# Optimization experiments

Measured on AMD Instinct MI355X. Metric: run time of the kernel, lower is better.

## Reference

```python
import jax, jax.numpy as jnp
import numpy as np

# Irreps 0e+1o+2e+3o: (name, dim); total irreps dim D = 1+3+5+7 = 16
IRS = [("0e", 1), ("1o", 3), ("2e", 5), ("3o", 7)]
D = 16
# path multiplicities per correlation order (MACE-like)
MULS = {3: [5, 8, 10, 10], 2: [2, 3, 4, 4], 1: [1, 1, 1, 1]}
NUM_RBF = 32
CHANNELS = 128
NUM_SPECIES = 64
BATCH = 256


def _make_U():
    # Sparse Clebsch-Gordan-like basis tensors: shape (D,)*order + (mul, ir_dim).
    # Stand-in for e3nn.reduced_symmetric_tensor_product_basis: deterministic,
    rng = np.random.default_rng(42)
    U = {}
    for order in (3, 2, 1):
        for (ir, dim), mul in zip(IRS, MULS[order]):
            shape = (D,) * order + (mul, dim)
            dense = rng.standard_normal(shape).astype(np.float32)
            mask = (rng.random(shape) < 0.1).astype(np.float32)
            U[(order, ir)] = jnp.asarray(dense * mask)
    return U

U_BASIS = _make_U()
WKEYS = [(o, ir) for o in (3, 2, 1) for ir, _ in IRS]


def setup_inputs() -> dict:
    key = jax.random.key(0)
    ks = jax.random.split(key, 16)
    inp = {
        "x": jax.random.normal(ks[0], (BATCH, CHANNELS, D), dtype=jnp.float32),
        "index": jax.random.randint(ks[1], (BATCH,), 0, NUM_SPECIES),
        "embed_table": jax.random.normal(ks[2], (NUM_SPECIES, NUM_RBF), dtype=jnp.float32),
    }
    i = 3
    for order in (3, 2, 1):
        for (ir, _), mul in zip(IRS, MULS[order]):
            inp[f"w{order}_{ir}"] = jax.random.normal(ks[i], (NUM_RBF, mul, CHANNELS), dtype=jnp.float32)
            i += 1
    return inp


def _forward(x, species_ind, Wd):
    # x: (b, c, D); species_ind: (b, num_rbf); Wd[(order, ir)]: (num_rbf, mul, c)
    out = {}
    fresh = set()
    for order in (3, 2, 1):
        for ir, _ in IRS:
            u = U_BASIS[(order, ir)] / order  # ((D,)*order, mul, ir_dim)
            # species-gathered per-channel path weights: (b, mul, c)
            w = jnp.einsum('be,ekc->bkc', species_ind, Wd[(order, ir)])
            if ir not in out:
                # highest order: contract one D axis with x, mul with w
                out[ir] = jnp.einsum('...jki,bkc,bcj->bc...i', u, w, x)
                fresh.add(ir)
            else:
                out[ir] = out[ir] + jnp.einsum('...ki,bkc->bc...i', u, w)
        for ir, _ in IRS:
            if ir in fresh:
                fresh.discard(ir)
                continue
            # contract one more D axis against x after each lower order
            out[ir] = jnp.einsum('bc...ji,bcj->bc...i', out[ir], x)
    # final per-ir shape (b, c, ir_dim); concat -> (b, c, D)
    return jnp.concatenate([out[ir] for ir, _ in IRS], axis=-1)


def reference(x, index, embed_table, w3_0e, w3_1o, w3_2e, w3_3o, w2_0e, w2_1o, w2_2e, w2_3o, w1_0e, w1_1o, w1_2e, w1_3o):
    ws = (w3_0e, w3_1o, w3_2e, w3_3o, w2_0e, w2_1o, w2_2e, w2_3o, w1_0e, w1_1o, w1_2e, w1_3o)
    Wd = {k: w for k, w in zip(WKEYS, ws)}
    species_ind = embed_table[index]  # (b, num_rbf) embedding lookup
    return _forward(x, species_ind, Wd)
```

## Files before the change

### kernel.cpp

```cpp
#include <hip/hip_runtime.h>
#include <cstdint>
#include <cmath>
#include <cstring>

#define D16    16
#define CH     128
#define NBATCH 256
#define NSP    64
#define NRBF   32
#define NKK    50
#define NT3    816
#define NT2    136
#define LD3    160
#define LD2    64
#define U3_FLOATS (NT3*LD3)
#define U2_FLOATS (NT2*LD2)
#define U1_FLOATS 256
#define U_TOTAL   (U3_FLOATS+U2_FLOATS+U1_FLOATS)

#define KPAD   1024
#define NPAD   256
#define NCH_REAL 61
#define RING   3

typedef __attribute__((ext_vector_type(8)))  short short8;
typedef __attribute__((ext_vector_type(16))) float f32x16;

__device__ uint16_t g_B[NPAD*KPAD];
__device__ float    g_ws[NSP*NKK*CH];
__device__ float    g_part[NBATCH*2*CH*D16];

__device__ __constant__ int8_t KK_ARR[NKK] = {
  0,0,0,0,0, 1,1,1,1,1,1,1,1, 2,2,2,2,2,2,2,2,2,2, 3,3,3,3,3,3,3,3,3,3,
  4,4, 5,5,5, 6,6,6,6, 7,7,7,7, 8,9,10,11 };
__device__ __constant__ int8_t KK_K[NKK] = {
  0,1,2,3,4, 0,1,2,3,4,5,6,7, 0,1,2,3,4,5,6,7,8,9, 0,1,2,3,4,5,6,7,8,9,
  0,1, 0,1,2, 0,1,2,3, 0,1,2,3, 0,0,0,0 };
__device__ __constant__ int8_t ARR_MUL[12] = {5,8,10,10, 2,3,4,4, 1,1,1,1};

struct WPtrs { const float* p[12]; };

struct TTab { uint8_t a0[KPAD]; uint8_t a1[KPAD]; uint8_t a2[KPAD]; };
constexpr TTab make_tab() {
  TTab t{};
  int i = 0;
  for (int A = 0; A < 16; ++A)
    for (int B = A; B < 16; ++B)
      for (int C = B; C < 16; ++C) { t.a0[i]=(uint8_t)A; t.a1[i]=(uint8_t)B; t.a2[i]=(uint8_t)C; ++i; }
  for (int A = 0; A < 16; ++A)
    for (int B = A; B < 16; ++B) { t.a0[i]=(uint8_t)A; t.a1[i]=(uint8_t)B; t.a2[i]=16; ++i; }
  for (int A = 0; A < 16; ++A) { t.a0[i]=(uint8_t)A; t.a1[i]=16; t.a2[i]=16; ++i; }
  for (; i < KPAD; ++i) { t.a0[i]=17; t.a1[i]=17; t.a2[i]=17; }
  return t;
}
static constexpr TTab TT = make_tab();

template<int K>
__device__ __forceinline__ float featK(const float (&xv)[16]) {
  constexpr int A = TT.a0[K], B = TT.a1[K], C = TT.a2[K];
  if constexpr (A == 17) { return 0.f; }
  else {
    float m = xv[A];
    if constexpr (B < 16) m *= xv[B];
    if constexpr (C < 16) m *= xv[C];
    return m;
  }
}

template<int K0>
__device__ __forceinline__ uint32_t pack2(const float (&xv)[16]) {
  if constexpr (TT.a0[K0] == 17 && TT.a0[K0+1] == 17) { return 0u; }
  else {
    float lo = featK<K0>(xv);
    float hi = featK<K0+1>(xv);
    uint32_t d;
    asm("v_cvt_pk_bf16_f32 %0, %1, %2" : "=v"(d) : "v"(lo), "v"(hi));
    return d;
  }
}

template<int CHUNK>
__device__ __forceinline__ short8 build_frag(const float (&xv)[16], bool kg_hi) {
  uint32_t pk0 = pack2<CHUNK*16 + 0>(xv);
  uint32_t pk1 = pack2<CHUNK*16 + 2>(xv);
  uint32_t pk2 = pack2<CHUNK*16 + 4>(xv);
  uint32_t pk3 = pack2<CHUNK*16 + 6>(xv);
  uint32_t pk4 = pack2<CHUNK*16 + 8>(xv);
  uint32_t pk5 = pack2<CHUNK*16 + 10>(xv);
  uint32_t pk6 = pack2<CHUNK*16 + 12>(xv);
  uint32_t pk7 = pack2<CHUNK*16 + 14>(xv);
  union { uint32_t u[4]; short8 s; } r;
  r.u[0] = kg_hi ? pk4 : pk0;
  r.u[1] = kg_hi ? pk5 : pk1;
  r.u[2] = kg_hi ? pk6 : pk2;
  r.u[3] = kg_hi ? pk7 : pk3;
  return r.s;
}

__device__ uint32_t colpack(int cc) {
  int kk, ii;
  if (cc < 149) {
    if (cc < 5)       { kk = cc;               ii = 0; }
    else if (cc < 29) { int r = cc-5;  kk = 5  + r/3; ii = 1 + r%3; }
    else if (cc < 79) { int r = cc-29; kk = 13 + r/5; ii = 4 + r%5; }
    else              { int r = cc-79; kk = 23 + r/7; ii = 9 + r%7; }
  } else if (cc < 208) {
    int j = cc - 149;
    if (j < 2)        { kk = 33 + j;           ii = 0; }
    else if (j < 11)  { int r = j-2;  kk = 35 + r/3; ii = 1 + r%3; }
    else if (j < 31)  { int r = j-11; kk = 38 + r/5; ii = 4 + r%5; }
    else              { int r = j-31; kk = 42 + r/7; ii = 9 + r%7; }
  } else {
    int j = cc - 208;
    if (j < 1)        { kk = 46; ii = 0; }
    else if (j < 4)   { kk = 47; ii = j; }
    else if (j < 9)   { kk = 48; ii = j; }
    else              { kk = 49; ii = j; }
  }
  return (uint32_t)((kk<<4) | ii);
}

__global__ void weights_kernel(const float* __restrict__ embed, WPtrs wp) {
  int kk = blockIdx.x;
  int s  = blockIdx.y;
  int c  = threadIdx.x;
  int ai = KK_ARR[kk];
  int k  = KK_K[kk];
  int mul = ARR_MUL[ai];
  const float* __restrict__ W = wp.p[ai];
  float a = 0.f;
  #pragma unroll 8
  for (int e = 0; e < NRBF; ++e)
    a = fmaf(embed[s*NRBF + e], W[(e*mul + k)*CH + c], a);
  g_ws[(s*NKK + kk)*CH + c] = a;
}

template<int C>
__device__ __forceinline__ void kstep(const float (&xv)[16], bool kg_hi,
                                      const uint16_t* __restrict__ pB,
                                      uint4 (&br0)[RING], uint4 (&br1)[RING],
                                      f32x16& a0, f32x16& a1) {
  union UU { uint4 u; short8 s; };
  UU b0; b0.u = br0[C % RING];
  UU b1; b1.u = br1[C % RING];
  short8 af = build_frag<C>(xv, kg_hi);
  a0 = __builtin_amdgcn_mfma_f32_32x32x16_bf16(af, b0.s, a0, 0, 0, 0);
  a1 = __builtin_amdgcn_mfma_f32_32x32x16_bf16(af, b1.s, a1, 0, 0, 0);
  if constexpr (C + RING < NCH_REAL) {
    br0[C % RING] = *(const uint4*)(pB + (size_t)(C+RING)*4096);
    br1[C % RING] = *(const uint4*)(pB + (size_t)(C+RING)*4096 + 256);
  }
}

__global__ __launch_bounds__(512, 2) void main_kernel(const float* __restrict__ x,
                                                      const int* __restrict__ index) {
  __shared__ float    out_lds[128*18];
  __shared__ uint32_t tab2[256];

  const int tid  = threadIdx.x;
  const int lane = tid & 63;
  const int l31  = lane & 31;
  const int kg   = lane >> 5;
  const bool kg_hi = (kg != 0);
  const int w    = tid >> 6;
  const int wmg  = w >> 1;
  const int wq   = w & 1;
  const int b    = blockIdx.x;
  const int nh   = blockIdx.y;
  const int s    = index[b];

  const int r0 = wmg*32 + l31;
  float xv[16];
  {
    const float4* xs = (const float4*)(x + ((size_t)b*CH + r0)*D16);
    #pragma unroll
    for (int qq = 0; qq < 4; ++qq) {
      float4 v = xs[qq];
      xv[qq*4+0]=v.x; xv[qq*4+1]=v.y; xv[qq*4+2]=v.z; xv[qq*4+3]=v.w;
    }
  }

  for (int i = tid; i < 128*18; i += 512) out_lds[i] = 0.f;
  if (tid < 256) tab2[tid] = (tid < 224) ? colpack(tid) : 0u;

  const uint16_t* __restrict__ pB = g_B + ((size_t)kg*256 + nh*128 + wq*64 + l31)*8;

  uint4 br0[RING], br1[RING];
  #pragma unroll
  for (int c = 0; c < RING; ++c) {
    br0[c] = *(const uint4*)(pB + (size_t)c*4096);
    br1[c] = *(const uint4*)(pB + (size_t)c*4096 + 256);
  }

  f32x16 a0, a1;
  #pragma unroll
  for (int q = 0; q < 16; ++q) { a0[q]=0.f; a1[q]=0.f; }

#define S1_(C) kstep<(C)>(xv, kg_hi, pB, br0, br1, a0, a1);
#define S4_(C) S1_(C) S1_(C+1) S1_(C+2) S1_(C+3)
  S4_(0)  S4_(4)  S4_(8)  S4_(12) S4_(16) S4_(20) S4_(24) S4_(28)
  S4_(32) S4_(36) S4_(40) S4_(44) S4_(48) S4_(52) S4_(56) S1_(60)
#undef S4_
#undef S1_

  __syncthreads();

#define FOLD(ACC, NT) { \
    int col = nh*128 + wq*64 + (NT)*32 + l31; \
    if (col < 224) { \
      uint32_t v = tab2[col]; \
      int kk = v >> 4, ii = v & 15; \
      const float* wsrow = g_ws + ((size_t)s*NKK + kk)*CH + wmg*32; \
      _Pragma("unroll") \
      for (int qg = 0; qg < 4; ++qg) { \
        int rlb = 8*qg + 4*kg; \
        float4 wv = *(const float4*)(wsrow + rlb); \
        int rbase = wmg*32 + rlb; \
        atomicAdd(&out_lds[(rbase + 0)*18 + ii], wv.x * (ACC)[qg*4+0]); \
        atomicAdd(&out_lds[(rbase + 1)*18 + ii], wv.y * (ACC)[qg*4+1]); \
        atomicAdd(&out_lds[(rbase + 2)*18 + ii], wv.z * (ACC)[qg*4+2]); \
        atomicAdd(&out_lds[(rbase + 3)*18 + ii], wv.w * (ACC)[qg*4+3]); \
      } \
    } }
  FOLD(a0, 0)
  FOLD(a1, 1)
#undef FOLD
  __syncthreads();

  { float* pp = g_part + ((size_t)b*2 + nh)*2048;
    int cch = tid >> 2, q = tid & 3;
    float4 o;
    o.x = out_lds[cch*18 + q*4 + 0];
    o.y = out_lds[cch*18 + q*4 + 1];
    o.z = out_lds[cch*18 + q*4 + 2];
    o.w = out_lds[cch*18 + q*4 + 3];
    *(float4*)(pp + cch*16 + q*4) = o; }
}

__global__ __launch_bounds__(512) void merge_kernel(float* __restrict__ out) {
  int idx = blockIdx.x*512 + threadIdx.x;
  size_t b   = (size_t)(idx >> 9);
  size_t off = (size_t)(idx & 511) * 4;
  const float4 p0 = *(const float4*)(g_part + b*4096 + off);
  const float4 p1 = *(const float4*)(g_part + b*4096 + 2048 + off);
  float4 o; o.x = p0.x+p1.x; o.y = p0.y+p1.y; o.z = p0.z+p1.z; o.w = p0.w+p1.w;
  *(float4*)(out + b*2048 + off) = o;
}

namespace host_rng {

typedef unsigned __int128 u128;

static inline u128 pcg_mult() {
  return (((u128)0x2360ed051fc65da4ULL) << 64) | 0x4385df649fccf645ULL;
}

struct PCG {
  u128 state, inc;
  inline uint64_t next() {
    state = state * pcg_mult() + inc;
    uint64_t hi = (uint64_t)(state >> 64), lo = (uint64_t)state;
    uint64_t x = hi ^ lo;
    unsigned rot = (unsigned)(hi >> 58);
    return (x >> rot) | (x << ((64u - rot) & 63u));
  }
  inline double nextd() { return (double)(next() >> 11) * (1.0 / 9007199254740992.0); }
};

static inline uint32_t hashmix(uint32_t v, uint32_t& hc) {
  v ^= hc; hc *= 0x931e8875u; v *= hc; v ^= v >> 16; return v;
}
static inline uint32_t mixfn(uint32_t x, uint32_t y) {
  uint32_t r = 0xca01f9ddu * x - 0x4973f715u * y; r ^= r >> 16; return r;
}

static void seed42(PCG& g) {
  uint32_t pool[4];
  uint32_t hc = 0x43b0d7e5u;
  pool[0] = hashmix(42u, hc);
  for (int i = 1; i < 4; ++i) pool[i] = hashmix(0u, hc);
  for (int si = 0; si < 4; ++si)
    for (int di = 0; di < 4; ++di)
      if (si != di) pool[di] = mixfn(pool[di], hashmix(pool[si], hc));
  uint32_t hb = 0x8b51f9ddu;
  uint32_t w32[8];
  for (int k = 0; k < 8; ++k) {
    uint32_t dv = pool[k & 3];
    dv ^= hb; hb *= 0x58f38dedu; dv *= hb; dv ^= dv >> 16;
    w32[k] = dv;
  }
  uint64_t s0 = (uint64_t)w32[0] | ((uint64_t)w32[1] << 32);
  uint64_t s1 = (uint64_t)w32[2] | ((uint64_t)w32[3] << 32);
  uint64_t s2 = (uint64_t)w32[4] | ((uint64_t)w32[5] << 32);
  uint64_t s3 = (uint64_t)w32[6] | ((uint64_t)w32[7] << 32);
  u128 initstate = ((u128)s0 << 64) | s1;
  u128 initseq   = ((u128)s2 << 64) | s3;
  g.inc   = (initseq << 1) | 1;
  g.state = g.inc;
  g.state += initstate;
  g.state = g.state * pcg_mult() + g.inc;
}

static double zig_w[256], zig_f[256];
static uint64_t zig_k[256];
static const double ZR = 3.6541528853610087963519472518;
static double ZRinv;

static void build_zig() {
  const double m1 = 4503599627370496.0;
  double fr   = std::exp(-0.5 * ZR * ZR);
  double tail = std::sqrt(M_PI * 0.5) * std::erfc(ZR / std::sqrt(2.0));
  double vn   = ZR * fr + tail;
  double q    = vn / fr;
  zig_k[0]   = (uint64_t)((ZR / q) * m1);
  zig_k[1]   = 0;
  zig_w[0]   = q / m1;
  zig_w[255] = ZR / m1;
  zig_f[0]   = 1.0;
  zig_f[255] = fr;
  double tn = ZR, dn = ZR;
  for (int i = 254; i >= 1; --i) {
    dn = std::sqrt(-2.0 * std::log(vn / dn + std::exp(-0.5 * dn * dn)));
    zig_k[i + 1] = (uint64_t)((dn / tn) * m1);
    tn = dn;
    zig_f[i] = std::exp(-0.5 * dn * dn);
    zig_w[i] = dn / m1;
  }
  ZRinv = 1.0 / ZR;
}

static double std_normal(PCG& g) {
  for (;;) {
    uint64_t r = g.next();
    int idx = (int)(r & 0xffu);
    r >>= 8;
    int sign = (int)(r & 1u);
    uint64_t rabs = (r >> 1) & 0x000fffffffffffffULL;
    double x = (double)rabs * zig_w[idx];
    if (sign) x = -x;
    if (rabs < zig_k[idx]) return x;
    if (idx == 0) {
      for (;;) {
        double xx = -ZRinv * std::log1p(-g.nextd());
        double yy = -std::log1p(-g.nextd());
        if (yy + yy > xx * xx)
          return ((rabs >> 8) & 1u) ? -(ZR + xx) : (ZR + xx);
      }
    } else {
      if ((zig_f[idx - 1] - zig_f[idx]) * g.nextd() + zig_f[idx] < std::exp(-0.5 * x * x))
        return x;
    }
  }
}

}

static float h_U[U_TOTAL];

static void build_U() {
  using namespace host_rng;
  build_zig();
  PCG g; seed42(g);

  static double S3[U3_FLOATS];
  static double S2[U2_FLOATS];
  static double S1[U1_FLOATS];
  std::memset(S3, 0, sizeof(S3));
  std::memset(S2, 0, sizeof(S2));
  std::memset(S1, 0, sizeof(S1));

  static int tmap[16][16][16];
  static int pmap[16][16];
  { int t = 0;
    for (int a0 = 0; a0 < 16; ++a0)
      for (int a1 = a0; a1 < 16; ++a1)
        for (int a2 = a1; a2 < 16; ++a2) tmap[a0][a1][a2] = t++; }
  { int t = 0;
    for (int a0 = 0; a0 < 16; ++a0)
      for (int a1 = a0; a1 < 16; ++a1) pmap[a0][a1] = t++; }

  const int muls3[4] = {5,8,10,10}, muls2[4] = {2,3,4,4};
  const int dims[4]  = {1,3,5,7};
  const int cb3[4]   = {0,5,29,79};
  const int cb2[4]   = {0,2,11,31};
  const int cb1[4]   = {0,1,4,9};

  static double nrm[16*16*16*10*7];

  for (int ir = 0; ir < 4; ++ir) {
    int mul = muls3[ir], dim = dims[ir];
    long n = 4096L * mul * dim;
    for (long j = 0; j < n; ++j) nrm[j] = std_normal(g);
    long j = 0;
    for (int a0 = 0; a0 < 16; ++a0)
      for (int a1 = 0; a1 < 16; ++a1)
        for (int a2 = 0; a2 < 16; ++a2) {
          int s0 = a0, s1 = a1, s2 = a2, tswap;
          if (s0 > s1) { tswap = s0; s0 = s1; s1 = tswap; }
          if (s1 > s2) { tswap = s1; s1 = s2; s2 = tswap; }
          if (s0 > s1) { tswap = s0; s0 = s1; s1 = tswap; }
          int t = tmap[s0][s1][s2];
          for (int k = 0; k < mul; ++k)
            for (int i = 0; i < dim; ++i, ++j) {
              double u = g.nextd();
              if (u < 0.1) {
                float v = (float)nrm[j];
                v = v / 3.0f;
                S3[t*LD3 + cb3[ir] + k*dim + i] += (double)v;
              }
            }
        }
  }
  for (int ir = 0; ir < 4; ++ir) {
    int mul = muls2[ir], dim = dims[ir];
    long n = 256L * mul * dim;
    for (long j = 0; j < n; ++j) nrm[j] = std_normal(g);
    long j = 0;
    for (int a0 = 0; a0 < 16; ++a0)
      for (int a1 = 0; a1 < 16; ++a1) {
        int s0 = a0 < a1 ? a0 : a1;
        int s1 = a0 < a1 ? a1 : a0;
        int t = pmap[s0][s1];
        for (int k = 0; k < mul; ++k)
          for (int i = 0; i < dim; ++i, ++j) {
            double u = g.nextd();
            if (u < 0.1) {
              float v = (float)nrm[j];
              v = v / 2.0f;
              S2[t*LD2 + cb2[ir] + k*dim + i] += (double)v;
            }
          }
      }
  }
  for (int ir = 0; ir < 4; ++ir) {
    int dim = dims[ir];
    long n = 16L * dim;
    for (long j = 0; j < n; ++j) nrm[j] = std_normal(g);
    long j = 0;
    for (int a0 = 0; a0 < 16; ++a0)
      for (int i = 0; i < dim; ++i, ++j) {
        double u = g.nextd();
        if (u < 0.1) {
          float v = (float)nrm[j];
          S1[a0*16 + cb1[ir] + i] += (double)v;
        }
      }
  }

  for (int i = 0; i < U3_FLOATS; ++i) h_U[i] = (float)S3[i];
  for (int i = 0; i < U2_FLOATS; ++i) h_U[U3_FLOATS + i] = (float)S2[i];
  for (int i = 0; i < U1_FLOATS; ++i) h_U[U3_FLOATS + U2_FLOATS + i] = (float)S1[i];
}

static uint16_t h_B_arr[NPAD*KPAD];
static const uint16_t* h_B_src = h_B_arr;

static inline uint16_t f2bf_h(float x) {
  uint32_t u; std::memcpy(&u, &x, 4);
  return (uint16_t)((u + 0x7fffu + ((u>>16)&1u)) >> 16);
}

static inline float Bval(int col, int k) {
  if (k < NT3)            { if (col < 149) return h_U[k*LD3 + col]; }
  else if (k < NT3+NT2)   { if (col >= 149 && col < 208) return h_U[U3_FLOATS + (k-NT3)*LD2 + (col-149)]; }
  else if (k < NT3+NT2+16){ if (col >= 208 && col < 224) return h_U[U3_FLOATS + U2_FLOATS + (k-(NT3+NT2))*16 + (col-208)]; }
  return 0.f;
}

struct UInit {
  UInit() {
    build_U();
    for (int c = 0; c < KPAD/16; ++c)
      for (int half = 0; half < 2; ++half)
        for (int col = 0; col < NPAD; ++col)
          for (int j = 0; j < 8; ++j) {
            int k = c*16 + half*8 + j;
            h_B_arr[((size_t)(c*2 + half)*NPAD + col)*8 + j] = f2bf_h(Bval(col, k));
          }
    void* p = nullptr;
    if (hipHostMalloc(&p, sizeof(h_B_arr), hipHostMallocDefault) == hipSuccess && p) {
      std::memcpy(p, h_B_arr, sizeof(h_B_arr));
      h_B_src = (const uint16_t*)p;
    }
  }
};
static UInit u_init_once;

extern "C" void kernel_launch(void* const* d_in, const int* in_sizes, int n_in,
                              void* d_out, int out_size, void* d_ws, size_t ws_size,
                              hipStream_t stream) {
  (void)in_sizes; (void)n_in; (void)d_ws; (void)ws_size; (void)out_size;

  const float* x     = (const float*)d_in[0];
  const int*   index = (const int*)d_in[1];
  const float* embed = (const float*)d_in[2];
  WPtrs wp;
  for (int i = 0; i < 12; ++i) wp.p[i] = (const float*)d_in[3 + i];

  void* bptr = nullptr;
  hipGetSymbolAddress(&bptr, HIP_SYMBOL(g_B));
  hipMemcpyAsync(bptr, h_B_src, sizeof(h_B_arr), hipMemcpyHostToDevice, stream);

  dim3 gw(NKK, NSP);
  weights_kernel<<<gw, CH, 0, stream>>>(embed, wp);
  dim3 gm(NBATCH, 2);
  main_kernel<<<gm, 512, 0, stream>>>(x, index);
  merge_kernel<<<256, 512, 0, stream>>>((float*)d_out);
}
```

Measured before the change: 97.15 us.

## Stage B operand through double-buffered LDS instead of per-wave register ring

The per-wave register prefetch ring of B fragments is replaced by cooperative block-wide loads into a double-buffered LDS tile. Each step stages four K-chunks and syncs the block. This cuts redundant global loads of B across the four row-group waves that share the same columns. In exchange it adds 16 block barriers, about 32KB of extra LDS per block (which may lower occupancy), and runs 64 K-chunks where the old loop ran 61.

```diff
diff --git a/kernel.cpp b/kernel.cpp
--- a/kernel.cpp
+++ b/kernel.cpp
@@ -20,8 +20,7 @@
 
 #define KPAD   1024
 #define NPAD   256
-#define NCH_REAL 61
-#define RING   3
+#define NSTEP  16
 
 typedef __attribute__((ext_vector_type(8)))  short short8;
 typedef __attribute__((ext_vector_type(16))) float f32x16;
@@ -135,25 +134,9 @@
   g_ws[(s*NKK + kk)*CH + c] = a;
 }
 
-template<int C>
-__device__ __forceinline__ void kstep(const float (&xv)[16], bool kg_hi,
-                                      const uint16_t* __restrict__ pB,
-                                      uint4 (&br0)[RING], uint4 (&br1)[RING],
-                                      f32x16& a0, f32x16& a1) {
-  union UU { uint4 u; short8 s; };
-  UU b0; b0.u = br0[C % RING];
-  UU b1; b1.u = br1[C % RING];
-  short8 af = build_frag<C>(xv, kg_hi);
-  a0 = __builtin_amdgcn_mfma_f32_32x32x16_bf16(af, b0.s, a0, 0, 0, 0);
-  a1 = __builtin_amdgcn_mfma_f32_32x32x16_bf16(af, b1.s, a1, 0, 0, 0);
-  if constexpr (C + RING < NCH_REAL) {
-    br0[C % RING] = *(const uint4*)(pB + (size_t)(C+RING)*4096);
-    br1[C % RING] = *(const uint4*)(pB + (size_t)(C+RING)*4096 + 256);
-  }
-}
-
 __global__ __launch_bounds__(512, 2) void main_kernel(const float* __restrict__ x,
                                                       const int* __restrict__ index) {
+  __shared__ uint16_t Bbuf[2][4][2][128][8];
   __shared__ float    out_lds[128*18];
   __shared__ uint32_t tab2[256];
 
@@ -163,13 +146,30 @@
   const int kg   = lane >> 5;
   const bool kg_hi = (kg != 0);
   const int w    = tid >> 6;
-  const int wmg  = w >> 1;
+  const int wm   = w >> 1;
   const int wq   = w & 1;
   const int b    = blockIdx.x;
   const int nh   = blockIdx.y;
   const int s    = index[b];
 
-  const int r0 = wmg*32 + l31;
+  const int scol = tid & 127;
+  const int skg  = (tid >> 7) & 1;
+  const int sch  = tid >> 8;
+  const uint16_t* __restrict__ gbase =
+      g_B + (size_t)skg*2048 + ((size_t)nh*128 + scol)*8;
+  const uint32_t ldsoff = (uint32_t)(skg*2048 + scol*16);
+  char* const bb = (char*)&Bbuf[0][0][0][0][0];
+
+  uint4 st0, st1;
+#define ISSUE(STEP) { \
+    st0 = *(const uint4*)(gbase + (size_t)((STEP)*4 + sch    )*4096); \
+    st1 = *(const uint4*)(gbase + (size_t)((STEP)*4 + sch + 2)*4096); }
+#define WRITE(NB) { \
+    *(uint4*)(bb + (NB)*16384 + (sch    )*4096 + ldsoff) = st0; \
+    *(uint4*)(bb + (NB)*16384 + (sch + 2)*4096 + ldsoff) = st1; }
+
+  ISSUE(0)
+  const int r0 = wm*32 + l31;
   float xv[16];
   {
     const float4* xs = (const float4*)(x + ((size_t)b*CH + r0)*D16);
@@ -179,43 +179,54 @@
       xv[qq*4+0]=v.x; xv[qq*4+1]=v.y; xv[qq*4+2]=v.z; xv[qq*4+3]=v.w;
     }
   }
-
   for (int i = tid; i < 128*18; i += 512) out_lds[i] = 0.f;
   if (tid < 256) tab2[tid] = (tid < 224) ? colpack(tid) : 0u;
-
-  const uint16_t* __restrict__ pB = g_B + ((size_t)kg*256 + nh*128 + wq*64 + l31)*8;
-
-  uint4 br0[RING], br1[RING];
-  #pragma unroll
-  for (int c = 0; c < RING; ++c) {
-    br0[c] = *(const uint4*)(pB + (size_t)c*4096);
-    br1[c] = *(const uint4*)(pB + (size_t)c*4096 + 256);
-  }
+  WRITE(0)
+  __syncthreads();
 
   f32x16 a0, a1;
   #pragma unroll
   for (int q = 0; q < 16; ++q) { a0[q]=0.f; a1[q]=0.f; }
 
-#define S1_(C) kstep<(C)>(xv, kg_hi, pB, br0, br1, a0, a1);
-#define S4_(C) S1_(C) S1_(C+1) S1_(C+2) S1_(C+3)
-  S4_(0)  S4_(4)  S4_(8)  S4_(12) S4_(16) S4_(20) S4_(24) S4_(28)
-  S4_(32) S4_(36) S4_(40) S4_(44) S4_(48) S4_(52) S4_(56) S1_(60)
-#undef S4_
-#undef S1_
-
-  __syncthreads();
+  const uint32_t boff = (uint32_t)(kg*2048 + (wq*64 + l31)*16);
+
+#define KCHUNK(C) { \
+    constexpr int CB_ = ((C) >> 2) & 1; \
+    constexpr int SL_ = (C) & 3; \
+    short8 af = build_frag<(C)>(xv, kg_hi); \
+    union UU { uint4 u; short8 s; } b0_, b1_; \
+    b0_.s = *(const short8*)(bb + CB_*16384 + SL_*4096 + boff); \
+    b1_.s = *(const short8*)(bb + CB_*16384 + SL_*4096 + boff + 512); \
+    a0 = __builtin_amdgcn_mfma_f32_32x32x16_bf16(af, b0_.s, a0, 0, 0, 0); \
+    a1 = __builtin_amdgcn_mfma_f32_32x32x16_bf16(af, b1_.s, a1, 0, 0, 0); }
+
+#define STEP(S) { \
+    if ((S) < NSTEP-1) ISSUE((S)+1) \
+    KCHUNK((S)*4+0) KCHUNK((S)*4+1) KCHUNK((S)*4+2) KCHUNK((S)*4+3) \
+    if ((S) < NSTEP-1) WRITE(((S)+1)&1) \
+    __syncthreads(); }
+
+  STEP(0)  STEP(1)  STEP(2)  STEP(3)
+  STEP(4)  STEP(5)  STEP(6)  STEP(7)
+  STEP(8)  STEP(9)  STEP(10) STEP(11)
+  STEP(12) STEP(13) STEP(14) STEP(15)
+
+#undef STEP
+#undef KCHUNK
+#undef WRITE
+#undef ISSUE
 
 #define FOLD(ACC, NT) { \
     int col = nh*128 + wq*64 + (NT)*32 + l31; \
     if (col < 224) { \
       uint32_t v = tab2[col]; \
       int kk = v >> 4, ii = v & 15; \
-      const float* wsrow = g_ws + ((size_t)s*NKK + kk)*CH + wmg*32; \
+      const float* wsrow = g_ws + ((size_t)s*NKK + kk)*CH + wm*32; \
       _Pragma("unroll") \
       for (int qg = 0; qg < 4; ++qg) { \
         int rlb = 8*qg + 4*kg; \
         float4 wv = *(const float4*)(wsrow + rlb); \
-        int rbase = wmg*32 + rlb; \
+        int rbase = wm*32 + rlb; \
         atomicAdd(&out_lds[(rbase + 0)*18 + ii], wv.x * (ACC)[qg*4+0]); \
         atomicAdd(&out_lds[(rbase + 1)*18 + ii], wv.y * (ACC)[qg*4+1]); \
         atomicAdd(&out_lds[(rbase + 2)*18 + ii], wv.z * (ACC)[qg*4+2]); \
```

After: 96.17 us. About the same (-1.0%).
